# Optimization experiments

Measured on AMD Instinct MI355X. Metric: run time of the kernel, lower is better.

Reference implementation:

```python
import jax, jax.numpy as jnp
import numpy as np

N_BITS = 3        # routing dims (slice_mask = first 3 indices)
N_HEADS = 8       # 2**N_BITS
D_FEAT = 512      # input_dim - N_BITS
D_BASE = 1024     # base MLP output
D_HEAD_H = 1024   # head hidden
D_OUT = 512       # head output
BATCH = 8192


def setup_inputs() -> dict:
    key = jax.random.key(0)
    ks = jax.random.split(key, 8)
    s = lambda fan_in: 1.0 / np.sqrt(fan_in)
    x = jax.random.normal(ks[0], (BATCH, N_BITS + D_FEAT), dtype=jnp.float32)
    Wb = jax.random.normal(ks[1], (D_FEAT, D_BASE), dtype=jnp.float32) * s(D_FEAT)
    bb = jax.random.normal(ks[2], (D_BASE,), dtype=jnp.float32) * s(D_FEAT)
    Wh1 = jax.random.normal(ks[3], (N_HEADS, D_BASE, D_HEAD_H), dtype=jnp.float32) * s(D_BASE)
    bh1 = jax.random.normal(ks[4], (N_HEADS, D_HEAD_H), dtype=jnp.float32) * s(D_BASE)
    Wh2 = jax.random.normal(ks[5], (N_HEADS, D_HEAD_H, D_OUT), dtype=jnp.float32) * s(D_HEAD_H)
    bh2 = jax.random.normal(ks[6], (N_HEADS, D_OUT), dtype=jnp.float32) * s(D_HEAD_H)
    return {"x": x, "Wb": Wb, "bb": bb, "Wh1": Wh1, "bh1": bh1, "Wh2": Wh2, "bh2": bh2}


def _combs():
    # Faithful to the torch `recursive` construction for three single-index
    # binary slices: combs[bit, head] = (head >> bit) & 1
    return ((jnp.arange(N_HEADS)[None, :] >> jnp.arange(N_BITS)[:, None]) & 1).astype(bool)


def reference(x, Wb, bb, Wh1, bh1, Wh2, bh2):
    bits = x[:, :N_BITS] > 0.5          # [B, 3] routing bits
    feat = x[:, N_BITS:]                # [B, 512]
    base = jax.nn.relu(feat @ Wb + bb)  # [B, 1024] shared base net
    # all heads run over the full batch (as in the original module)
    h = jax.nn.relu(jnp.einsum('bd,hde->bhe', base, Wh1) + bh1[None])  # [B, 8, 1024]
    out_all = jnp.einsum('bhe,heo->bho', h, Wh2) + bh2[None]           # [B, 8, 512]
    combs = _combs()                                                   # [3, 8]
    sel = jnp.all(bits[:, :, None] == combs[None], axis=1).astype(x.dtype)  # [B, 8] one-hot
    return jnp.einsum('bho,bh->bo', out_all, sel)                      # [B, 512]
```

## Files before the change

### kernel.cpp

```cpp
#include <hip/hip_runtime.h>
#include <hip/hip_bf16.h>
#include <stdint.h>

using short8 = __attribute__((ext_vector_type(8))) short;
using f32x4  = __attribute__((ext_vector_type(4))) float;

#define NBITS 3
#define NHEADS 8
#define BATCH 8192
#define DFEAT 512
#define DBASE 1024
#define DHH   1024
#define DOUT  512
#define XCOLS (NBITS + DFEAT)

static __device__ __forceinline__ unsigned short f2bf(float f) {
    union { float f; unsigned u; } v; v.f = f;
    unsigned r = v.u + 0x7FFFu + ((v.u >> 16) & 1u);
    return (unsigned short)(r >> 16);
}

__global__ void k_bucket(const float* __restrict__ x, int* __restrict__ cnt,
                         int* __restrict__ rows) {
    int r = blockIdx.x * 256 + threadIdx.x;
    if (r >= BATCH) return;
    const float* xr = x + (size_t)r * XCOLS;
    int h = (xr[0] > 0.5f ? 1 : 0) | (xr[1] > 0.5f ? 2 : 0) | (xr[2] > 0.5f ? 4 : 0);
    int slot = atomicAdd(cnt + h, 1);
    rows[h * BATCH + slot] = r;
}

__global__ void k_feat(const float* __restrict__ x, unsigned short* __restrict__ feat) {
    int t = blockIdx.x * 256 + threadIdx.x;
    int row = t >> 6, c8 = (t & 63) << 3;
    const float* src = x + (size_t)row * XCOLS + NBITS + c8;
    short8 v;
#pragma unroll
    for (int i = 0; i < 8; ++i) v[i] = (short)f2bf(src[i]);
    *(short8*)(feat + (size_t)row * DFEAT + c8) = v;
}

__global__ void k_transpose(const float* __restrict__ W, unsigned short* __restrict__ WT,
                            int K, int N) {
    __shared__ float tile[32][33];
    int b  = blockIdx.z;
    int n0 = blockIdx.x << 5, k0 = blockIdx.y << 5;
    int tx = threadIdx.x & 31, ty = threadIdx.x >> 5;
    const float* Wb = W + (size_t)b * K * N;
    unsigned short* WTb = WT + (size_t)b * K * N;
#pragma unroll
    for (int j = 0; j < 32; j += 8)
        tile[ty + j][tx] = Wb[(size_t)(k0 + ty + j) * N + n0 + tx];
    __syncthreads();
#pragma unroll
    for (int j = 0; j < 32; j += 8)
        WTb[(size_t)(n0 + ty + j) * K + k0 + tx] = f2bf(tile[tx][ty + j]);
}

template<bool GATHER, bool RELU, bool OUTBF16, int NF>
__global__ __launch_bounds__(256, 2)
void k_gemmd(const unsigned short* __restrict__ A, int lda, int K,
             const unsigned short* __restrict__ BT,
             const float* __restrict__ bias,
             void* __restrict__ C, int ldc,
             const int* __restrict__ rowsAll, const int* __restrict__ cntAll,
             int Nfull, int nshift) {
    constexpr int BN = NF * 16 * 4;
    const int bid  = blockIdx.x;
    const int mt   = bid & 127;
    const int nt   = (bid >> 7) & ((1 << nshift) - 1);
    const int head = GATHER ? (bid >> (7 + nshift)) : 0;
    const int m0 = mt * 64;
    const int n0 = nt * BN;
    int M = BATCH;
    const int* rows = nullptr;
    if (GATHER) {
        M = cntAll[head];
        if (m0 >= M) return;
        rows = rowsAll + head * BATCH;
    }
    const unsigned short* BTh = BT + (size_t)head * Nfull * K;
    const float* biash = bias + (size_t)head * Nfull;

    __shared__ __align__(16) char lds[2 * 32768];

    const int t    = threadIdx.x;
    const int w    = t >> 6;
    const int lane = t & 63;
    const int ln = lane & 15, lq = lane >> 4;
    const int r7 = ln & 7;

    const unsigned short* gsrc[8];
#pragma unroll
    for (int i = 0; i < 8; ++i) {
        int r  = i * 8 + (t >> 5);
        int lg = (t & 31) ^ (r & 7);
        int gr;
        if (GATHER) { int idx = m0 + r; idx = idx < M ? idx : M - 1; gr = rows[idx]; }
        else gr = m0 + r;
        gsrc[i] = A + (size_t)gr * lda + lg * 8;
    }
    const unsigned short* gb[NF];
#pragma unroll
    for (int n = 0; n < NF; ++n) {
        int col = n0 + w * (NF * 16) + n * 16 + ln;
        gb[n] = BTh + (size_t)col * K + lq * 8;
    }
    const int dstw = w * 1024;

#define STAGEQ(cq_, d_)                                                                    \
    { _Pragma("unroll") for (int i = 0; i < 8; ++i)                                        \
        __builtin_amdgcn_global_load_lds(                                                  \
            (const __attribute__((address_space(1))) void*)(gsrc[i] + (cq_) * 256),        \
            (__attribute__((address_space(3))) void*)(lds + (d_) * 32768 + i * 4096 + dstw), \
            16, 0, 0); }

    f32x4 acc[4][NF] = {};
    const int NC = K >> 8;

    STAGEQ(0, 0);
    __syncthreads();

    for (int cq = 0; cq < NC; ++cq) {
        const int d = cq & 1;
        if (cq + 1 < NC) STAGEQ(cq + 1, d ^ 1);
        const char* cA = lds + d * 32768;
        const unsigned short* bq[NF];
#pragma unroll
        for (int n = 0; n < NF; ++n) bq[n] = gb[n] + cq * 256;
#pragma unroll
        for (int ks = 0; ks < 8; ++ks) {
            short8 af[4], bf[NF];
#pragma unroll
            for (int m = 0; m < 4; ++m) {
                int row  = m * 16 + ln;
                int phys = ((ks * 4) | lq) ^ r7;
                af[m] = *(const short8*)(cA + row * 512 + phys * 16);
            }
#pragma unroll
            for (int n = 0; n < NF; ++n)
                bf[n] = *(const short8*)(bq[n] + ks * 32);
#pragma unroll
            for (int m = 0; m < 4; ++m)
#pragma unroll
                for (int n = 0; n < NF; ++n)
                    acc[m][n] = __builtin_amdgcn_mfma_f32_16x16x32_bf16(af[m], bf[n], acc[m][n], 0, 0, 0);
        }
        __syncthreads();
    }
#undef STAGEQ

#pragma unroll
    for (int n = 0; n < NF; ++n) {
        int col = n0 + w * (NF * 16) + n * 16 + ln;
        float bv = biash[col];
#pragma unroll
        for (int m = 0; m < 4; ++m) {
#pragma unroll
            for (int j = 0; j < 4; ++j) {
                int rt = m * 16 + lq * 4 + j;
                int grow;
                if (GATHER) {
                    if (m0 + rt >= M) continue;
                    grow = rows[m0 + rt];
                } else {
                    grow = m0 + rt;
                }
                float v = acc[m][n][j] + bv;
                if (RELU) v = fmaxf(v, 0.0f);
                if (OUTBF16)
                    ((unsigned short*)C)[(size_t)grow * ldc + col] = f2bf(v);
                else
                    ((float*)C)[(size_t)grow * ldc + col] = v;
            }
        }
    }
}

extern "C" void kernel_launch(void* const* d_in, const int* in_sizes, int n_in,
                              void* d_out, int out_size, void* d_ws, size_t ws_size,
                              hipStream_t stream) {
    const float* x   = (const float*)d_in[0];
    const float* Wb  = (const float*)d_in[1];
    const float* bb  = (const float*)d_in[2];
    const float* Wh1 = (const float*)d_in[3];
    const float* bh1 = (const float*)d_in[4];
    const float* Wh2 = (const float*)d_in[5];
    const float* bh2 = (const float*)d_in[6];

    char* ws = (char*)d_ws;
    unsigned short* feat = (unsigned short*)(ws);
    unsigned short* WbT  = (unsigned short*)(ws + (8ull  << 20));
    unsigned short* Wh1T = (unsigned short*)(ws + (9ull  << 20));
    unsigned short* Wh2T = (unsigned short*)(ws + (25ull << 20));
    unsigned short* base = (unsigned short*)(ws + (33ull << 20));
    unsigned short* hbuf = (unsigned short*)(ws + (49ull << 20));
    int* rows            = (int*)(ws + (65ull << 20));
    int* cnt             = (int*)(ws + (65ull << 20) + (256ull << 10));

    hipMemsetAsync(cnt, 0, NHEADS * sizeof(int), stream);
    k_bucket<<<BATCH / 256, 256, 0, stream>>>(x, cnt, rows);
    k_feat<<<(BATCH * 64) / 256, 256, 0, stream>>>(x, feat);
    k_transpose<<<dim3(DBASE / 32, DFEAT / 32, 1), 256, 0, stream>>>(Wb, WbT, DFEAT, DBASE);
    k_transpose<<<dim3(DHH / 32, DBASE / 32, NHEADS), 256, 0, stream>>>(Wh1, Wh1T, DBASE, DHH);
    k_transpose<<<dim3(DOUT / 32, DHH / 32, NHEADS), 256, 0, stream>>>(Wh2, Wh2T, DHH, DOUT);

    k_gemmd<false, true, true, 4><<<512, 256, 0, stream>>>(
        feat, DFEAT, DFEAT, WbT, bb, base, DBASE, nullptr, nullptr, DBASE, 2);
    k_gemmd<true, true, true, 4><<<4096, 256, 0, stream>>>(
        base, DBASE, DBASE, Wh1T, bh1, hbuf, DHH, rows, cnt, DHH, 2);
    k_gemmd<true, false, false, 2><<<4096, 256, 0, stream>>>(
        hbuf, DHH, DHH, Wh2T, bh2, d_out, DOUT, rows, cnt, DOUT, 2);
}
```

Baseline: 354.9 us.

## Fuse per-head hidden and output GEMMs into one kernel keeping hidden tile in LDS

Replaces the two separate gathered head GEMMs with a single kernel that, per 32-row tile of a head's routed rows, computes the hidden layer into LDS and then immediately multiplies by the second head weight. This removes the global round-trip of the hidden activations and one launch. The base GEMM is specialized with constant dimensions. The tradeoff is a smaller M tile (32 rows) with 512 threads and 128KB of LDS, so occupancy drops to one block per CU and weight reuse per tile is lower. Weights are read directly from global memory per wave.

```diff
diff --git a/kernel.cpp b/kernel.cpp
--- a/kernel.cpp
+++ b/kernel.cpp
@@ -57,30 +57,16 @@
         WTb[(size_t)(n0 + ty + j) * K + k0 + tx] = f2bf(tile[tx][ty + j]);
 }
 
-template<bool GATHER, bool RELU, bool OUTBF16, int NF>
 __global__ __launch_bounds__(256, 2)
-void k_gemmd(const unsigned short* __restrict__ A, int lda, int K,
+void k_gemm1(const unsigned short* __restrict__ A,
              const unsigned short* __restrict__ BT,
              const float* __restrict__ bias,
-             void* __restrict__ C, int ldc,
-             const int* __restrict__ rowsAll, const int* __restrict__ cntAll,
-             int Nfull, int nshift) {
-    constexpr int BN = NF * 16 * 4;
-    const int bid  = blockIdx.x;
-    const int mt   = bid & 127;
-    const int nt   = (bid >> 7) & ((1 << nshift) - 1);
-    const int head = GATHER ? (bid >> (7 + nshift)) : 0;
+             unsigned short* __restrict__ C) {
+    const int bid = blockIdx.x;
+    const int nt  = bid & 3;
+    const int mt  = bid >> 2;
     const int m0 = mt * 64;
-    const int n0 = nt * BN;
-    int M = BATCH;
-    const int* rows = nullptr;
-    if (GATHER) {
-        M = cntAll[head];
-        if (m0 >= M) return;
-        rows = rowsAll + head * BATCH;
-    }
-    const unsigned short* BTh = BT + (size_t)head * Nfull * K;
-    const float* biash = bias + (size_t)head * Nfull;
+    const int n0 = nt * 256;
 
     __shared__ __align__(16) char lds[2 * 32768];
 
@@ -95,16 +81,13 @@
     for (int i = 0; i < 8; ++i) {
         int r  = i * 8 + (t >> 5);
         int lg = (t & 31) ^ (r & 7);
-        int gr;
-        if (GATHER) { int idx = m0 + r; idx = idx < M ? idx : M - 1; gr = rows[idx]; }
-        else gr = m0 + r;
-        gsrc[i] = A + (size_t)gr * lda + lg * 8;
-    }
-    const unsigned short* gb[NF];
-#pragma unroll
-    for (int n = 0; n < NF; ++n) {
-        int col = n0 + w * (NF * 16) + n * 16 + ln;
-        gb[n] = BTh + (size_t)col * K + lq * 8;
+        gsrc[i] = A + (size_t)(m0 + r) * DFEAT + lg * 8;
+    }
+    const unsigned short* gb[4];
+#pragma unroll
+    for (int n = 0; n < 4; ++n) {
+        int col = n0 + w * 64 + n * 16 + ln;
+        gb[n] = BT + (size_t)col * DFEAT + lq * 8;
     }
     const int dstw = w * 1024;
 
@@ -115,22 +98,18 @@
             (__attribute__((address_space(3))) void*)(lds + (d_) * 32768 + i * 4096 + dstw), \
             16, 0, 0); }
 
-    f32x4 acc[4][NF] = {};
-    const int NC = K >> 8;
-
+    f32x4 acc[4][4] = {};
     STAGEQ(0, 0);
     __syncthreads();
 
-    for (int cq = 0; cq < NC; ++cq) {
+#pragma unroll 1
+    for (int cq = 0; cq < 2; ++cq) {
         const int d = cq & 1;
-        if (cq + 1 < NC) STAGEQ(cq + 1, d ^ 1);
+        if (cq == 0) STAGEQ(1, 1);
         const char* cA = lds + d * 32768;
-        const unsigned short* bq[NF];
-#pragma unroll
-        for (int n = 0; n < NF; ++n) bq[n] = gb[n] + cq * 256;
 #pragma unroll
         for (int ks = 0; ks < 8; ++ks) {
-            short8 af[4], bf[NF];
+            short8 af[4], bf[4];
 #pragma unroll
             for (int m = 0; m < 4; ++m) {
                 int row  = m * 16 + ln;
@@ -138,12 +117,12 @@
                 af[m] = *(const short8*)(cA + row * 512 + phys * 16);
             }
 #pragma unroll
-            for (int n = 0; n < NF; ++n)
-                bf[n] = *(const short8*)(bq[n] + ks * 32);
+            for (int n = 0; n < 4; ++n)
+                bf[n] = *(const short8*)(gb[n] + cq * 256 + ks * 32);
 #pragma unroll
             for (int m = 0; m < 4; ++m)
 #pragma unroll
-                for (int n = 0; n < NF; ++n)
+                for (int n = 0; n < 4; ++n)
                     acc[m][n] = __builtin_amdgcn_mfma_f32_16x16x32_bf16(af[m], bf[n], acc[m][n], 0, 0, 0);
         }
         __syncthreads();
@@ -151,29 +130,140 @@
 #undef STAGEQ
 
 #pragma unroll
-    for (int n = 0; n < NF; ++n) {
-        int col = n0 + w * (NF * 16) + n * 16 + ln;
-        float bv = biash[col];
-#pragma unroll
-        for (int m = 0; m < 4; ++m) {
+    for (int n = 0; n < 4; ++n) {
+        int col = n0 + w * 64 + n * 16 + ln;
+        float bv = bias[col];
+#pragma unroll
+        for (int m = 0; m < 4; ++m)
+#pragma unroll
+            for (int j = 0; j < 4; ++j) {
+                int row = m0 + m * 16 + lq * 4 + j;
+                float v = fmaxf(acc[m][n][j] + bv, 0.0f);
+                C[(size_t)row * DBASE + col] = f2bf(v);
+            }
+    }
+}
+
+__global__ __launch_bounds__(512, 1)
+void k_fused23(const unsigned short* __restrict__ base,
+               const unsigned short* __restrict__ Wh1T,
+               const float* __restrict__ bh1,
+               const unsigned short* __restrict__ Wh2T,
+               const float* __restrict__ bh2,
+               float* __restrict__ out,
+               const int* __restrict__ rowsAll, const int* __restrict__ cntAll) {
+    const int bid  = blockIdx.x;
+    const int head = bid >> 7;
+    const int mt   = bid & 127;
+    const int M  = cntAll[head];
+    const int m0 = mt * 32;
+    if (m0 >= M) return;
+    const int* rows = rowsAll + head * BATCH + m0;
+    const int nrows = (M - m0) < 32 ? (M - m0) : 32;
+
+    __shared__ __align__(16) char ldsA[65536];
+    __shared__ __align__(16) char ldsH[65536];
+
+    const int t = threadIdx.x, w = t >> 6, lane = t & 63;
+    const int ln = lane & 15, lq = lane >> 4;
+
+#pragma unroll
+    for (int i = 0; i < 8; ++i) {
+        int id   = i * 512 + t;
+        int r    = id >> 7;
+        int phys = id & 127;
+        int lg   = phys ^ (r & 7);
+        int rr   = r < nrows ? r : nrows - 1;
+        const unsigned short* src = base + (size_t)rows[rr] * DBASE + lg * 8;
+        __builtin_amdgcn_global_load_lds(
+            (const __attribute__((address_space(1))) void*)src,
+            (__attribute__((address_space(3))) void*)(ldsA + i * 8192 + w * 1024),
+            16, 0, 0);
+    }
+    asm volatile("s_waitcnt vmcnt(0)" ::: "memory");
+    __builtin_amdgcn_s_barrier();
+
+    const unsigned short* W1 = Wh1T + (size_t)head * DHH * DBASE;
+    const float* b1 = bh1 + head * DHH;
+#pragma unroll 1
+    for (int s = 0; s < 4; ++s) {
+        const int cbase = s * 256 + w * 32;
+        f32x4 acc[2][2];
+#pragma unroll
+        for (int nf = 0; nf < 2; ++nf) {
+            float bv = b1[cbase + nf * 16 + ln];
+#pragma unroll
+            for (int m = 0; m < 2; ++m) acc[m][nf] = (f32x4){bv, bv, bv, bv};
+        }
+        const unsigned short* w1p[2];
+#pragma unroll
+        for (int nf = 0; nf < 2; ++nf)
+            w1p[nf] = W1 + (size_t)(cbase + nf * 16 + ln) * DBASE + lq * 8;
+#pragma unroll 4
+        for (int ks = 0; ks < 32; ++ks) {
+            int phys = ((ks * 4 + lq) ^ (ln & 7)) * 16;
+            short8 a0 = *(const short8*)(ldsA + ln * 2048 + phys);
+            short8 a1 = *(const short8*)(ldsA + (16 + ln) * 2048 + phys);
+            short8 b0 = *(const short8*)(w1p[0] + ks * 32);
+            short8 bv1 = *(const short8*)(w1p[1] + ks * 32);
+            acc[0][0] = __builtin_amdgcn_mfma_f32_16x16x32_bf16(a0, b0,  acc[0][0], 0, 0, 0);
+            acc[1][0] = __builtin_amdgcn_mfma_f32_16x16x32_bf16(a1, b0,  acc[1][0], 0, 0, 0);
+            acc[0][1] = __builtin_amdgcn_mfma_f32_16x16x32_bf16(a0, bv1, acc[0][1], 0, 0, 0);
+            acc[1][1] = __builtin_amdgcn_mfma_f32_16x16x32_bf16(a1, bv1, acc[1][1], 0, 0, 0);
+        }
+#pragma unroll
+        for (int nf = 0; nf < 2; ++nf)
+#pragma unroll
+            for (int m = 0; m < 2; ++m)
+#pragma unroll
+                for (int j = 0; j < 4; ++j) {
+                    int row = m * 16 + lq * 4 + j;
+                    int col = cbase + nf * 16 + ln;
+                    float v = fmaxf(acc[m][nf][j], 0.0f);
+                    int phys = (col >> 3) ^ (row & 7);
+                    *(unsigned short*)(ldsH + row * 2048 + phys * 16 + (col & 7) * 2) = f2bf(v);
+                }
+    }
+    __syncthreads();
+
+    const unsigned short* W2 = Wh2T + (size_t)head * DOUT * DHH;
+    const float* b2 = bh2 + head * DOUT;
+    f32x4 acc3[2][4];
+    const unsigned short* w2p[4];
+#pragma unroll
+    for (int nf = 0; nf < 4; ++nf) {
+        int col = w * 64 + nf * 16 + ln;
+        float bv = b2[col];
+        acc3[0][nf] = (f32x4){bv, bv, bv, bv};
+        acc3[1][nf] = (f32x4){bv, bv, bv, bv};
+        w2p[nf] = W2 + (size_t)col * DHH + lq * 8;
+    }
+#pragma unroll 4
+    for (int ks = 0; ks < 32; ++ks) {
+        int phys = ((ks * 4 + lq) ^ (ln & 7)) * 16;
+        short8 a0 = *(const short8*)(ldsH + ln * 2048 + phys);
+        short8 a1 = *(const short8*)(ldsH + (16 + ln) * 2048 + phys);
+        short8 bf[4];
+#pragma unroll
+        for (int nf = 0; nf < 4; ++nf)
+            bf[nf] = *(const short8*)(w2p[nf] + ks * 32);
+#pragma unroll
+        for (int nf = 0; nf < 4; ++nf) {
+            acc3[0][nf] = __builtin_amdgcn_mfma_f32_16x16x32_bf16(a0, bf[nf], acc3[0][nf], 0, 0, 0);
+            acc3[1][nf] = __builtin_amdgcn_mfma_f32_16x16x32_bf16(a1, bf[nf], acc3[1][nf], 0, 0, 0);
+        }
+    }
+#pragma unroll
+    for (int nf = 0; nf < 4; ++nf) {
+        int col = w * 64 + nf * 16 + ln;
+#pragma unroll
+        for (int m = 0; m < 2; ++m)
 #pragma unroll
             for (int j = 0; j < 4; ++j) {
                 int rt = m * 16 + lq * 4 + j;
-                int grow;
-                if (GATHER) {
-                    if (m0 + rt >= M) continue;
-                    grow = rows[m0 + rt];
-                } else {
-                    grow = m0 + rt;
-                }
-                float v = acc[m][n][j] + bv;
-                if (RELU) v = fmaxf(v, 0.0f);
-                if (OUTBF16)
-                    ((unsigned short*)C)[(size_t)grow * ldc + col] = f2bf(v);
-                else
-                    ((float*)C)[(size_t)grow * ldc + col] = v;
+                if (rt < nrows)
+                    out[(size_t)rows[rt] * DOUT + col] = acc3[m][nf][j];
             }
-        }
     }
 }
 
@@ -194,9 +284,8 @@
     unsigned short* Wh1T = (unsigned short*)(ws + (9ull  << 20));
     unsigned short* Wh2T = (unsigned short*)(ws + (25ull << 20));
     unsigned short* base = (unsigned short*)(ws + (33ull << 20));
-    unsigned short* hbuf = (unsigned short*)(ws + (49ull << 20));
-    int* rows            = (int*)(ws + (65ull << 20));
-    int* cnt             = (int*)(ws + (65ull << 20) + (256ull << 10));
+    int* rows            = (int*)(ws + (49ull << 20));
+    int* cnt             = (int*)(ws + (49ull << 20) + (256ull << 10));
 
     hipMemsetAsync(cnt, 0, NHEADS * sizeof(int), stream);
     k_bucket<<<BATCH / 256, 256, 0, stream>>>(x, cnt, rows);
@@ -205,10 +294,7 @@
     k_transpose<<<dim3(DHH / 32, DBASE / 32, NHEADS), 256, 0, stream>>>(Wh1, Wh1T, DBASE, DHH);
     k_transpose<<<dim3(DOUT / 32, DHH / 32, NHEADS), 256, 0, stream>>>(Wh2, Wh2T, DHH, DOUT);
 
-    k_gemmd<false, true, true, 4><<<512, 256, 0, stream>>>(
-        feat, DFEAT, DFEAT, WbT, bb, base, DBASE, nullptr, nullptr, DBASE, 2);
-    k_gemmd<true, true, true, 4><<<4096, 256, 0, stream>>>(
-        base, DBASE, DBASE, Wh1T, bh1, hbuf, DHH, rows, cnt, DHH, 2);
-    k_gemmd<true, false, false, 2><<<4096, 256, 0, stream>>>(
-        hbuf, DHH, DHH, Wh2T, bh2, d_out, DOUT, rows, cnt, DOUT, 2);
-}
+    k_gemm1<<<512, 256, 0, stream>>>(feat, WbT, bb, base);
+    k_fused23<<<1024, 512, 0, stream>>>(base, Wh1T, bh1, Wh2T, bh2,
+                                        (float*)d_out, rows, cnt);
+}
```

New measurement: 371.9 us. 1.05x slower.
